# Optimization experiments

Hardware: AMD Instinct MI355X
Metric: run time of the kernel (lower is better)

## Reference

```python
import jax, jax.numpy as jnp
import numpy as np

MODEL_DIM = 1024
NUM_HEADS = 16
HEAD_DIM = MODEL_DIM // NUM_HEADS


def setup_inputs() -> dict:
    key = jax.random.key(0)
    ks = jax.random.split(key, 9)
    s = 1.0 / np.sqrt(MODEL_DIM)
    d = {
        "query": jax.random.normal(ks[0], (2, 2048, MODEL_DIM), dtype=jnp.float32),
        "Wq": jax.random.normal(ks[1], (MODEL_DIM, MODEL_DIM), dtype=jnp.float32) * s,
        "bq": jnp.zeros((MODEL_DIM,), dtype=jnp.float32),
        "Wk": jax.random.normal(ks[2], (MODEL_DIM, MODEL_DIM), dtype=jnp.float32) * s,
        "bk": jnp.zeros((MODEL_DIM,), dtype=jnp.float32),
        "Wv": jax.random.normal(ks[3], (MODEL_DIM, MODEL_DIM), dtype=jnp.float32) * s,
        "bv": jnp.zeros((MODEL_DIM,), dtype=jnp.float32),
        "Wo": jax.random.normal(ks[4], (MODEL_DIM, MODEL_DIM), dtype=jnp.float32) * s,
        "bo": jnp.zeros((MODEL_DIM,), dtype=jnp.float32),
    }
    return d


def reference(query, Wq, bq, Wk, bk, Wv, bv, Wo, bo):
    B, S, D = query.shape
    H, hd = NUM_HEADS, HEAD_DIM
    # self-attention: key = value = query
    q = (query @ Wq.T + bq).reshape(B, S, H, hd).transpose(0, 2, 1, 3)  # [B,H,S,hd]
    k = (query @ Wk.T + bk).reshape(B, S, H, hd).transpose(0, 2, 1, 3)
    v = (query @ Wv.T + bv).reshape(B, S, H, hd).transpose(0, 2, 1, 3)
    scores = jnp.einsum("bhqd,bhkd->bhqk", q, k) / np.sqrt(hd)  # [B,H,S,S]
    attn = jax.nn.softmax(scores, axis=-1)
    ctx = jnp.einsum("bhqk,bhkd->bhqd", attn, v)  # [B,H,S,hd]
    ctx = ctx.transpose(0, 2, 1, 3).reshape(B, S, D)
    return ctx @ Wo.T + bo
```

## Files before the change

### kernel.cpp

```cpp
#include <hip/hip_runtime.h>

typedef __attribute__((ext_vector_type(8))) __bf16 bf16x8;
typedef __attribute__((ext_vector_type(8))) unsigned short ushort8;
typedef __attribute__((ext_vector_type(4))) unsigned short ushort4v;
typedef __attribute__((ext_vector_type(4))) float f32x4;
typedef __attribute__((ext_vector_type(2))) _Float16 f16x2;
typedef __attribute__((ext_vector_type(4))) _Float16 f16x4;
typedef __attribute__((ext_vector_type(8))) _Float16 f16x8;
typedef __attribute__((ext_vector_type(2))) __fp16 fp16v2;

__device__ __forceinline__ unsigned short f2bf(float f) {
    union { float f; unsigned int u; } c; c.f = f;
    unsigned int u = c.u;
    u += 0x7fffu + ((u >> 16) & 1u);
    return (unsigned short)(u >> 16);
}

__device__ __forceinline__ void async16(const void* g, void* l) {
    __builtin_amdgcn_global_load_lds(
        (const __attribute__((address_space(1))) unsigned int*)g,
        (__attribute__((address_space(3))) unsigned int*)l, 16, 0, 0);
}

__global__ __launch_bounds__(256) void cvt_all(
    const float* __restrict__ q,  const float* __restrict__ wq,
    const float* __restrict__ wk, const float* __restrict__ wv,
    const float* __restrict__ wo,
    unsigned short* __restrict__ q_bf, unsigned short* __restrict__ wqkv,
    unsigned short* __restrict__ wo_bf, float scale_k)
{
    const int NQ = 4096 * 1024, NW = 1024 * 1024;
    int i = (blockIdx.x * 256 + threadIdx.x) * 4;
    const float* src; unsigned short* dst; float sc = 1.0f; int off;
    if (i < NQ)               { src = q;  dst = q_bf;          off = i; }
    else if (i < NQ + NW)     { src = wq; dst = wqkv;          off = i - NQ; }
    else if (i < NQ + 2 * NW) { src = wk; dst = wqkv + NW;     off = i - NQ - NW; sc = scale_k; }
    else if (i < NQ + 3 * NW) { src = wv; dst = wqkv + 2 * NW; off = i - NQ - 2 * NW; }
    else                      { src = wo; dst = wo_bf;         off = i - NQ - 3 * NW; }
    float4 v = *(const float4*)(src + off);
    ushort4v o;
    o[0] = f2bf(v.x * sc); o[1] = f2bf(v.y * sc);
    o[2] = f2bf(v.z * sc); o[3] = f2bf(v.w * sc);
    *(ushort4v*)(dst + off) = o;
}

__global__ __launch_bounds__(256) void qkv_gemm(
    const unsigned short* __restrict__ A,
    const unsigned short* __restrict__ B,
    unsigned short* __restrict__ qkv,
    _Float16* __restrict__ vtg,
    const float* __restrict__ b0, const float* __restrict__ b1, const float* __restrict__ b2,
    float s1)
{
    __shared__ __align__(16) unsigned short As[128 * 64];
    __shared__ __align__(16) unsigned short Bs[128 * 64];

    const int tid  = threadIdx.x;
    const int lane = tid & 63, wave = tid >> 6;
    const int quad = lane >> 4, l15 = lane & 15;
    const int wm = wave >> 1, wn = wave & 1;
    const int by = blockIdx.y, bx = blockIdx.x;
    const int K = 1024;

    const int srow = lane >> 3;
    const int sp   = lane & 7;
    const int scl  = sp ^ srow;
    const int sw   = l15 & 7;

    f32x4 acc[4][4];
#pragma unroll
    for (int i = 0; i < 4; ++i)
#pragma unroll
        for (int j = 0; j < 4; ++j) acc[i][j] = (f32x4)(0.0f);

    for (int kt = 0; kt < 16; ++kt) {
        __syncthreads();
#pragma unroll
        for (int j = 0; j < 4; ++j) {
            int r0 = wave * 32 + j * 8;
            async16(A + (size_t)(by * 128 + r0 + srow) * K + kt * 64 + scl * 8, &As[r0 * 64]);
            async16(B + (size_t)(bx * 128 + r0 + srow) * K + kt * 64 + scl * 8, &Bs[r0 * 64]);
        }
        __syncthreads();

#pragma unroll
        for (int kh = 0; kh < 2; ++kh) {
            bf16x8 af[4], bfr[4];
#pragma unroll
            for (int mi = 0; mi < 4; ++mi)
                af[mi] = __builtin_bit_cast(bf16x8,
                    *(const ushort8*)&As[(wm * 64 + mi * 16 + l15) * 64 + ((kh * 4 + quad) ^ sw) * 8]);
#pragma unroll
            for (int ni = 0; ni < 4; ++ni)
                bfr[ni] = __builtin_bit_cast(bf16x8,
                    *(const ushort8*)&Bs[(wn * 64 + ni * 16 + l15) * 64 + ((kh * 4 + quad) ^ sw) * 8]);
#pragma unroll
            for (int mi = 0; mi < 4; ++mi)
#pragma unroll
                for (int ni = 0; ni < 4; ++ni)
                    acc[mi][ni] = __builtin_amdgcn_mfma_f32_16x16x32_bf16(af[mi], bfr[ni], acc[mi][ni], 0, 0, 0);
        }
    }

    if (bx < 16) {
#pragma unroll
        for (int ni = 0; ni < 4; ++ni) {
            int n = bx * 128 + wn * 64 + ni * 16 + l15;
            float bias = (n < 1024) ? b0[n] : b1[n - 1024] * s1;
#pragma unroll
            for (int mi = 0; mi < 4; ++mi) {
#pragma unroll
                for (int r = 0; r < 4; ++r) {
                    int m = by * 128 + wm * 64 + mi * 16 + quad * 4 + r;
                    qkv[(size_t)m * 2048 + n] = f2bf(acc[mi][ni][r] + bias);
                }
            }
        }
    } else {
        const int mb = by * 128 + wm * 64;
        const int b  = mb >> 11;
        const int st = (mb & 2047) >> 6;
#pragma unroll
        for (int ni = 0; ni < 4; ++ni) {
            int vf = (bx - 16) * 128 + wn * 64 + ni * 16 + l15;
            int h = vf >> 6, hd = vf & 63;
            float bias = b2[vf];
            _Float16* vrow = vtg + ((size_t)((b * 16 + h) * 64 + hd)) * 2048 + st * 64;
#pragma unroll
            for (int mi = 0; mi < 4; ++mi) {
                int p = ((mi >> 1) * 4 + quad) ^ (l15 & 7);
                f16x4 o;
#pragma unroll
                for (int r = 0; r < 4; ++r) o[r] = (_Float16)(acc[mi][ni][r] + bias);
                *(f16x4*)(vrow + p * 8 + (mi & 1) * 4) = o;
            }
        }
    }
}

__global__ __launch_bounds__(256) void out_gemm(
    const unsigned short* __restrict__ A,
    const unsigned short* __restrict__ B,
    float* __restrict__ Cout,
    const float* __restrict__ bo)
{
    __shared__ __align__(16) unsigned short As[128 * 64];
    __shared__ __align__(16) unsigned short Bs[64 * 64];

    const int tid  = threadIdx.x;
    const int lane = tid & 63, wave = tid >> 6;
    const int quad = lane >> 4, l15 = lane & 15;
    const int wm = wave >> 1, wn = wave & 1;
    const int by = blockIdx.y, bx = blockIdx.x;
    const int K = 1024;

    const int srow = lane >> 3;
    const int sp   = lane & 7;
    const int scl  = sp ^ srow;
    const int sw   = l15 & 7;

    f32x4 acc[4][2];
#pragma unroll
    for (int i = 0; i < 4; ++i)
#pragma unroll
        for (int j = 0; j < 2; ++j) acc[i][j] = (f32x4)(0.0f);

    for (int kt = 0; kt < 16; ++kt) {
        __syncthreads();
#pragma unroll
        for (int j = 0; j < 4; ++j) {
            int r0 = wave * 32 + j * 8;
            async16(A + (size_t)(by * 128 + r0 + srow) * K + kt * 64 + scl * 8, &As[r0 * 64]);
        }
#pragma unroll
        for (int j = 0; j < 2; ++j) {
            int r0 = wave * 16 + j * 8;
            async16(B + (size_t)(bx * 64 + r0 + srow) * K + kt * 64 + scl * 8, &Bs[r0 * 64]);
        }
        __syncthreads();

#pragma unroll
        for (int kh = 0; kh < 2; ++kh) {
            bf16x8 af[4], bfr[2];
#pragma unroll
            for (int mi = 0; mi < 4; ++mi)
                af[mi] = __builtin_bit_cast(bf16x8,
                    *(const ushort8*)&As[(wm * 64 + mi * 16 + l15) * 64 + ((kh * 4 + quad) ^ sw) * 8]);
#pragma unroll
            for (int ni = 0; ni < 2; ++ni)
                bfr[ni] = __builtin_bit_cast(bf16x8,
                    *(const ushort8*)&Bs[(wn * 32 + ni * 16 + l15) * 64 + ((kh * 4 + quad) ^ sw) * 8]);
#pragma unroll
            for (int mi = 0; mi < 4; ++mi)
#pragma unroll
                for (int ni = 0; ni < 2; ++ni)
                    acc[mi][ni] = __builtin_amdgcn_mfma_f32_16x16x32_bf16(af[mi], bfr[ni], acc[mi][ni], 0, 0, 0);
        }
    }

#pragma unroll
    for (int ni = 0; ni < 2; ++ni) {
        int n = bx * 64 + wn * 32 + ni * 16 + l15;
        float bias = bo[n];
#pragma unroll
        for (int mi = 0; mi < 4; ++mi) {
#pragma unroll
            for (int r = 0; r < 4; ++r) {
                int m = by * 128 + wm * 64 + mi * 16 + quad * 4 + r;
                Cout[(size_t)m * 1024 + n] = acc[mi][ni][r] + bias;
            }
        }
    }
}

struct KSet { bf16x8 f[4][2]; };

__device__ __forceinline__ void loadK(const unsigned short* __restrict__ qkv,
                                      int b, int h, int kt, int l15, int quad, KSet& ks) {
#pragma unroll
    for (int mt = 0; mt < 4; ++mt) {
        const unsigned short* kr =
            qkv + (size_t)(b * 2048 + kt * 64 + mt * 16 + l15) * 2048 + 1024 + h * 64;
        ks.f[mt][0] = __builtin_bit_cast(bf16x8, *(const ushort8*)(kr + quad * 8));
        ks.f[mt][1] = __builtin_bit_cast(bf16x8, *(const ushort8*)(kr + 32 + quad * 8));
    }
}

__global__ __launch_bounds__(256, 2) void attn(const unsigned short* __restrict__ qkv,
                                               const _Float16* __restrict__ vtg,
                                               unsigned short* __restrict__ ctx)
{
    __shared__ __align__(16) char smem[65536];

    const int tid  = threadIdx.x;
    const int lane = tid & 63, wave = tid >> 6;
    const int quad = lane >> 4, l15 = lane & 15;
    const int bh = blockIdx.y;
    const int b = bh >> 4, h = bh & 15;
    const int q0 = blockIdx.x * 64;

    const int srow = lane >> 3;
    const int sp   = lane & 7;
    const int sw   = l15 & 7;

    _Float16* VtW[2] = { (_Float16*)(smem + wave * 16384),
                         (_Float16*)(smem + wave * 16384 + 8192) };

    bf16x8 qf[4][2];
#pragma unroll
    for (int s = 0; s < 4; ++s) {
        int qrow = b * 2048 + q0 + s * 16 + l15;
#pragma unroll
        for (int kh = 0; kh < 2; ++kh)
            qf[s][kh] = __builtin_bit_cast(bf16x8,
                *(const ushort8*)(qkv + (size_t)qrow * 2048 + h * 64 + kh * 32 + quad * 8));
    }

    f32x4 ot[4][4];
#pragma unroll
    for (int s = 0; s < 4; ++s)
#pragma unroll
        for (int ht = 0; ht < 4; ++ht) ot[s][ht] = (f32x4)(0.0f);
    float l_acc[4] = {0.0f, 0.0f, 0.0f, 0.0f};
    const fp16v2 ones = {(__fp16)1.0f, (__fp16)1.0f};

    auto issueV = [&](int t, int vb) {
#pragma unroll
        for (int j = 0; j < 8; ++j) {
            int row = j * 8 + srow;
            async16(vtg + (size_t)(bh * 64 + row) * 2048 + (wave * 8 + t) * 64 + sp * 8,
                    (unsigned short*)&VtW[vb][j * 8 * 64]);
        }
    };

    auto computeTile = [&](const KSet& ks, const _Float16* Vt) {
        f16x4 pv[4][4];
#pragma unroll
        for (int mt = 0; mt < 4; ++mt) {
#pragma unroll
            for (int s = 0; s < 4; ++s) {
                f32x4 s4 = (f32x4)(0.0f);
                s4 = __builtin_amdgcn_mfma_f32_16x16x32_bf16(ks.f[mt][0], qf[s][0], s4, 0, 0, 0);
                s4 = __builtin_amdgcn_mfma_f32_16x16x32_bf16(ks.f[mt][1], qf[s][1], s4, 0, 0, 0);
                float p0 = __builtin_amdgcn_exp2f(s4[0]);
                float p1 = __builtin_amdgcn_exp2f(s4[1]);
                float p2 = __builtin_amdgcn_exp2f(s4[2]);
                float p3 = __builtin_amdgcn_exp2f(s4[3]);
                fp16v2 lo = __builtin_amdgcn_cvt_pkrtz(p0, p1);
                fp16v2 hi = __builtin_amdgcn_cvt_pkrtz(p2, p3);
                l_acc[s] = __builtin_amdgcn_fdot2(lo, ones, l_acc[s], false);
                l_acc[s] = __builtin_amdgcn_fdot2(hi, ones, l_acc[s], false);
                f16x2 lo2 = __builtin_bit_cast(f16x2, lo);
                f16x2 hi2 = __builtin_bit_cast(f16x2, hi);
                pv[s][mt] = __builtin_shufflevector(lo2, hi2, 0, 1, 2, 3);
            }
        }
#pragma unroll
        for (int ht = 0; ht < 4; ++ht) {
            const _Float16* vb = &Vt[(ht * 16 + l15) * 64];
#pragma unroll
            for (int g = 0; g < 2; ++g) {
                f16x8 v8 = *(const f16x8*)(vb + (((g * 4 + quad) ^ sw)) * 8);
                f16x4 vlo = __builtin_shufflevector(v8, v8, 0, 1, 2, 3);
                f16x4 vhi = __builtin_shufflevector(v8, v8, 4, 5, 6, 7);
#pragma unroll
                for (int s = 0; s < 4; ++s) {
                    ot[s][ht] = __builtin_amdgcn_mfma_f32_16x16x16f16(vlo, pv[s][2 * g],     ot[s][ht], 0, 0, 0);
                    ot[s][ht] = __builtin_amdgcn_mfma_f32_16x16x16f16(vhi, pv[s][2 * g + 1], ot[s][ht], 0, 0, 0);
                }
            }
        }
    };

    KSet kA, kB;
    issueV(0, 0);
    loadK(qkv, b, h, wave * 8 + 0, l15, quad, kA);

    for (int tt = 0; tt < 4; ++tt) {
        issueV(2 * tt + 1, 1);
        loadK(qkv, b, h, wave * 8 + 2 * tt + 1, l15, quad, kB);
        asm volatile("s_waitcnt vmcnt(16)" ::: "memory");
        __builtin_amdgcn_sched_barrier(0);
        computeTile(kA, VtW[0]);

        if (tt < 3) {
            issueV(2 * tt + 2, 0);
            loadK(qkv, b, h, wave * 8 + 2 * tt + 2, l15, quad, kA);
            asm volatile("s_waitcnt vmcnt(16)" ::: "memory");
        } else {
            asm volatile("s_waitcnt vmcnt(0)" ::: "memory");
        }
        __builtin_amdgcn_sched_barrier(0);
        computeTile(kB, VtW[1]);
    }

    float lred[4];
#pragma unroll
    for (int s = 0; s < 4; ++s) {
        float l = l_acc[s];
        l += __shfl_xor(l, 16, 64);
        l += __shfl_xor(l, 32, 64);
        lred[s] = l;
    }

    __syncthreads();
    float* lsh = (float*)smem;
    if (quad == 0) {
#pragma unroll
        for (int s = 0; s < 4; ++s) lsh[wave * 64 + s * 16 + l15] = lred[s];
    }
    __syncthreads();
    int myrow = wave * 16 + l15;
    float lt = lsh[0 * 64 + myrow] + lsh[1 * 64 + myrow] + lsh[2 * 64 + myrow] + lsh[3 * 64 + myrow];
    float inv = 1.0f / lt;

    __syncthreads();
    float* red = (float*)smem;
#pragma unroll
    for (int s = 0; s < 4; ++s) {
#pragma unroll
        for (int ht = 0; ht < 4; ++ht) {
            int c = (ht * 4 + quad) ^ l15;
            *(f32x4*)(red + wave * 4096 + (s * 16 + l15) * 64 + c * 4) = ot[s][ht];
        }
    }
    __syncthreads();
    {
        int qrow = b * 2048 + q0 + myrow;
#pragma unroll
        for (int ht = 0; ht < 4; ++ht) {
            int c = (ht * 4 + quad) ^ l15;
            f32x4 ssum = *(const f32x4*)(red + 0 * 4096 + myrow * 64 + c * 4);
#pragma unroll
            for (int w2 = 1; w2 < 4; ++w2)
                ssum += *(const f32x4*)(red + w2 * 4096 + myrow * 64 + c * 4);
            ushort4v o4;
#pragma unroll
            for (int r = 0; r < 4; ++r) o4[r] = f2bf(ssum[r] * inv);
            *(ushort4v*)(ctx + (size_t)qrow * 1024 + h * 64 + ht * 16 + quad * 4) = o4;
        }
    }
}

extern "C" void kernel_launch(void* const* d_in, const int* in_sizes, int n_in,
                              void* d_out, int out_size, void* d_ws, size_t ws_size,
                              hipStream_t stream) {
    const float* query = (const float*)d_in[0];
    const float* Wq = (const float*)d_in[1];
    const float* bq = (const float*)d_in[2];
    const float* Wk = (const float*)d_in[3];
    const float* bk = (const float*)d_in[4];
    const float* Wv = (const float*)d_in[5];
    const float* bv = (const float*)d_in[6];
    const float* Wo = (const float*)d_in[7];
    const float* bo = (const float*)d_in[8];

    char* ws = (char*)d_ws;
    unsigned short* q_bf  = (unsigned short*)(ws);
    unsigned short* ctx   = (unsigned short*)(ws);
    unsigned short* wqkv  = (unsigned short*)(ws + 8388608);
    unsigned short* wo_bf = (unsigned short*)(ws + 14680064);
    unsigned short* qkv   = (unsigned short*)(ws + 16777216);
    _Float16*       vtg   = (_Float16*)(ws + 33554432);

    const float SCALE = 0.125f * 1.4426950408889634f;

    cvt_all<<<8192, 256, 0, stream>>>(query, Wq, Wk, Wv, Wo, q_bf, wqkv, wo_bf, SCALE);
    qkv_gemm<<<dim3(24, 32), 256, 0, stream>>>(q_bf, wqkv, qkv, vtg, bq, bk, bv, SCALE);
    attn<<<dim3(32, 32), 256, 0, stream>>>(qkv, vtg, ctx);
    out_gemm<<<dim3(16, 32), 256, 0, stream>>>(ctx, wo_bf, (float*)d_out, bo);
}
```

Before: 218.5 us.

## Restructure attention loop to single K register set with split QK/PV phases

Splits each tile's compute into a QK/softmax phase and a PV phase. The next K tile is loaded into the same register set right after the QK phase, and the next V tile is issued into the LDS buffer that PV has just finished reading. This drops the second KSet register buffer to ease register pressure at two blocks per CU. The cost is a shorter prefetch distance for K, so K load latency may be less well hidden.

```diff
diff --git a/kernel.cpp b/kernel.cpp
--- a/kernel.cpp
+++ b/kernel.cpp
@@ -243,8 +243,8 @@
     const int sp   = lane & 7;
     const int sw   = l15 & 7;
 
-    _Float16* VtW[2] = { (_Float16*)(smem + wave * 16384),
-                         (_Float16*)(smem + wave * 16384 + 8192) };
+    _Float16* VA = (_Float16*)(smem + wave * 16384);
+    _Float16* VB = (_Float16*)(smem + wave * 16384 + 8192);
 
     bf16x8 qf[4][2];
 #pragma unroll
@@ -264,75 +264,84 @@
     float l_acc[4] = {0.0f, 0.0f, 0.0f, 0.0f};
     const fp16v2 ones = {(__fp16)1.0f, (__fp16)1.0f};
 
-    auto issueV = [&](int t, int vb) {
-#pragma unroll
-        for (int j = 0; j < 8; ++j) {
-            int row = j * 8 + srow;
-            async16(vtg + (size_t)(bh * 64 + row) * 2048 + (wave * 8 + t) * 64 + sp * 8,
-                    (unsigned short*)&VtW[vb][j * 8 * 64]);
-        }
-    };
-
-    auto computeTile = [&](const KSet& ks, const _Float16* Vt) {
-        f16x4 pv[4][4];
-#pragma unroll
-        for (int mt = 0; mt < 4; ++mt) {
-#pragma unroll
-            for (int s = 0; s < 4; ++s) {
-                f32x4 s4 = (f32x4)(0.0f);
-                s4 = __builtin_amdgcn_mfma_f32_16x16x32_bf16(ks.f[mt][0], qf[s][0], s4, 0, 0, 0);
-                s4 = __builtin_amdgcn_mfma_f32_16x16x32_bf16(ks.f[mt][1], qf[s][1], s4, 0, 0, 0);
-                float p0 = __builtin_amdgcn_exp2f(s4[0]);
-                float p1 = __builtin_amdgcn_exp2f(s4[1]);
-                float p2 = __builtin_amdgcn_exp2f(s4[2]);
-                float p3 = __builtin_amdgcn_exp2f(s4[3]);
-                fp16v2 lo = __builtin_amdgcn_cvt_pkrtz(p0, p1);
-                fp16v2 hi = __builtin_amdgcn_cvt_pkrtz(p2, p3);
-                l_acc[s] = __builtin_amdgcn_fdot2(lo, ones, l_acc[s], false);
-                l_acc[s] = __builtin_amdgcn_fdot2(hi, ones, l_acc[s], false);
-                f16x2 lo2 = __builtin_bit_cast(f16x2, lo);
-                f16x2 hi2 = __builtin_bit_cast(f16x2, hi);
-                pv[s][mt] = __builtin_shufflevector(lo2, hi2, 0, 1, 2, 3);
-            }
-        }
-#pragma unroll
-        for (int ht = 0; ht < 4; ++ht) {
-            const _Float16* vb = &Vt[(ht * 16 + l15) * 64];
-#pragma unroll
-            for (int g = 0; g < 2; ++g) {
-                f16x8 v8 = *(const f16x8*)(vb + (((g * 4 + quad) ^ sw)) * 8);
-                f16x4 vlo = __builtin_shufflevector(v8, v8, 0, 1, 2, 3);
-                f16x4 vhi = __builtin_shufflevector(v8, v8, 4, 5, 6, 7);
-#pragma unroll
-                for (int s = 0; s < 4; ++s) {
-                    ot[s][ht] = __builtin_amdgcn_mfma_f32_16x16x16f16(vlo, pv[s][2 * g],     ot[s][ht], 0, 0, 0);
-                    ot[s][ht] = __builtin_amdgcn_mfma_f32_16x16x16f16(vhi, pv[s][2 * g + 1], ot[s][ht], 0, 0, 0);
-                }
-            }
-        }
-    };
-
-    KSet kA, kB;
-    issueV(0, 0);
+#define ISSUEV(t, Vbuf) do {                                                          \
+    _Pragma("unroll")                                                                 \
+    for (int j = 0; j < 8; ++j) {                                                     \
+        int row = j * 8 + srow;                                                       \
+        async16(vtg + (size_t)(bh * 64 + row) * 2048 + (wave * 8 + (t)) * 64 + sp * 8,\
+                (unsigned short*)&(Vbuf)[j * 8 * 64]);                                \
+    } } while (0)
+
+#define QK_PHASE() do {                                                               \
+    _Pragma("unroll")                                                                 \
+    for (int mt = 0; mt < 4; ++mt) {                                                  \
+        _Pragma("unroll")                                                             \
+        for (int s = 0; s < 4; ++s) {                                                 \
+            f32x4 s4 = (f32x4)(0.0f);                                                 \
+            s4 = __builtin_amdgcn_mfma_f32_16x16x32_bf16(kA.f[mt][0], qf[s][0], s4, 0, 0, 0); \
+            s4 = __builtin_amdgcn_mfma_f32_16x16x32_bf16(kA.f[mt][1], qf[s][1], s4, 0, 0, 0); \
+            float p0 = __builtin_amdgcn_exp2f(s4[0]);                                 \
+            float p1 = __builtin_amdgcn_exp2f(s4[1]);                                 \
+            float p2 = __builtin_amdgcn_exp2f(s4[2]);                                 \
+            float p3 = __builtin_amdgcn_exp2f(s4[3]);                                 \
+            fp16v2 lo = __builtin_amdgcn_cvt_pkrtz(p0, p1);                           \
+            fp16v2 hi = __builtin_amdgcn_cvt_pkrtz(p2, p3);                           \
+            l_acc[s] = __builtin_amdgcn_fdot2(lo, ones, l_acc[s], false);             \
+            l_acc[s] = __builtin_amdgcn_fdot2(hi, ones, l_acc[s], false);             \
+            f16x2 lo2 = __builtin_bit_cast(f16x2, lo);                                \
+            f16x2 hi2 = __builtin_bit_cast(f16x2, hi);                                \
+            pv[s][mt] = __builtin_shufflevector(lo2, hi2, 0, 1, 2, 3);                \
+        }                                                                             \
+    } } while (0)
+
+#define PV_PHASE(Vbuf) do {                                                           \
+    _Pragma("unroll")                                                                 \
+    for (int ht = 0; ht < 4; ++ht) {                                                  \
+        const _Float16* vb = &(Vbuf)[(ht * 16 + l15) * 64];                           \
+        _Pragma("unroll")                                                             \
+        for (int g = 0; g < 2; ++g) {                                                 \
+            f16x8 v8 = *(const f16x8*)(vb + (((g * 4 + quad) ^ sw)) * 8);             \
+            f16x4 vlo = __builtin_shufflevector(v8, v8, 0, 1, 2, 3);                  \
+            f16x4 vhi = __builtin_shufflevector(v8, v8, 4, 5, 6, 7);                  \
+            _Pragma("unroll")                                                         \
+            for (int s = 0; s < 4; ++s) {                                             \
+                ot[s][ht] = __builtin_amdgcn_mfma_f32_16x16x16f16(vlo, pv[s][2 * g],     ot[s][ht], 0, 0, 0); \
+                ot[s][ht] = __builtin_amdgcn_mfma_f32_16x16x16f16(vhi, pv[s][2 * g + 1], ot[s][ht], 0, 0, 0); \
+            }                                                                         \
+        }                                                                             \
+    } } while (0)
+
+    KSet kA;
+    ISSUEV(0, VA);
     loadK(qkv, b, h, wave * 8 + 0, l15, quad, kA);
+    ISSUEV(1, VB);
 
     for (int tt = 0; tt < 4; ++tt) {
-        issueV(2 * tt + 1, 1);
-        loadK(qkv, b, h, wave * 8 + 2 * tt + 1, l15, quad, kB);
-        asm volatile("s_waitcnt vmcnt(16)" ::: "memory");
-        __builtin_amdgcn_sched_barrier(0);
-        computeTile(kA, VtW[0]);
-
-        if (tt < 3) {
-            issueV(2 * tt + 2, 0);
-            loadK(qkv, b, h, wave * 8 + 2 * tt + 2, l15, quad, kA);
+        {
+            f16x4 pv[4][4];
+            QK_PHASE();
+            loadK(qkv, b, h, wave * 8 + 2 * tt + 1, l15, quad, kA);
             asm volatile("s_waitcnt vmcnt(16)" ::: "memory");
-        } else {
-            asm volatile("s_waitcnt vmcnt(0)" ::: "memory");
-        }
-        __builtin_amdgcn_sched_barrier(0);
-        computeTile(kB, VtW[1]);
-    }
+            __builtin_amdgcn_sched_barrier(0);
+            PV_PHASE(VA);
+            __builtin_amdgcn_sched_barrier(0);
+            if (tt < 3) ISSUEV(2 * tt + 2, VA);
+        }
+        {
+            f16x4 pv[4][4];
+            QK_PHASE();
+            if (tt < 3) loadK(qkv, b, h, wave * 8 + 2 * tt + 2, l15, quad, kA);
+            asm volatile("s_waitcnt vmcnt(16)" ::: "memory");
+            __builtin_amdgcn_sched_barrier(0);
+            PV_PHASE(VB);
+            __builtin_amdgcn_sched_barrier(0);
+            if (tt < 3) ISSUEV(2 * tt + 3, VB);
+        }
+    }
+
+#undef ISSUEV
+#undef QK_PHASE
+#undef PV_PHASE
 
     float lred[4];
 #pragma unroll
```

Measured after the change: 204.4 us. 1.07x faster.
